# Optimization experiments

Hardware: AMD Instinct MI355X
Metric: run time of the kernel (lower is better)

The kernel has to match this reference:

```python
import jax, jax.numpy as jnp
import numpy as np

N, DEG, F_IN, F_OUT, H = 8192, 16, 1024, 128, 8


def setup_inputs() -> dict:
    key = jax.random.key(0)
    ks = jax.random.split(key, 6)
    features = jax.random.normal(ks[0], (N, F_IN), dtype=jnp.float32)
    adj = jax.random.randint(ks[1], (N, DEG), 0, N)  # fixed-degree adjacency
    W = jax.random.normal(ks[2], (H, F_IN, F_OUT), dtype=jnp.float32) / np.sqrt(F_IN)
    bW = jax.random.normal(ks[3], (H, F_OUT), dtype=jnp.float32) * 0.01
    a = jax.random.normal(ks[4], (H, 2 * F_OUT), dtype=jnp.float32) / np.sqrt(2.0 * F_OUT)
    ba = jax.random.normal(ks[5], (H,), dtype=jnp.float32) * 0.01
    return {"features": features, "adj": adj, "W": W, "bW": bW, "a": a, "ba": ba}


def reference(features, adj, W, bW, a, ba):
    n = features.shape[0]
    # neighbors with self appended last (matches adjlist[node] + [node])
    nbr = jnp.concatenate([adj, jnp.arange(n)[:, None]], axis=1)  # [N, DEG+1]
    # per-head linear transform: h[k] = features @ W_k + b_k
    h = jnp.einsum('nf,hfo->hno', features, W) + bW[:, None, :]  # [H, N, F_OUT]
    # attention score a_k([h_dst, h_src]) + bias decomposed into dst/src parts
    a_dst, a_src = a[:, :F_OUT], a[:, F_OUT:]
    s_dst = jnp.einsum('hno,ho->hn', h, a_dst)  # [H, N]
    s_src = jnp.einsum('hno,ho->hn', h, a_src)  # [H, N]
    scores = s_dst[:, :, None] + s_src[:, nbr] + ba[:, None, None]  # [H, N, DEG+1]
    scores = jax.nn.leaky_relu(scores, 0.2)
    alpha = jax.nn.softmax(scores, axis=-1)  # softmax over neighbors (incl. self)
    h_src = h[:, nbr]  # [H, N, DEG+1, F_OUT]
    out = jnp.einsum('hnd,hndf->hnf', alpha, h_src)  # [H, N, F_OUT]
    # concat heads along feature dim -> [N, H*F_OUT]
    return out.transpose(1, 0, 2).reshape(n, H * F_OUT)
```

## Files before the change

### kernel.cpp

```cpp
#include <hip/hip_runtime.h>
#include <hip/hip_bf16.h>

#define N_NODES 8192
#define DEG     16
#define F_IN    1024
#define F_OUT   128
#define NH      8

typedef __bf16 bf16x8 __attribute__((ext_vector_type(8)));
typedef float  f32x4  __attribute__((ext_vector_type(4)));

__device__ __forceinline__ float bf2f(unsigned short u) {
    union { unsigned int i; float f; } v;
    v.i = ((unsigned int)u) << 16;
    return v.f;
}
__device__ __forceinline__ unsigned short f2bf(float f) {
    union { float f; unsigned int u; } v; v.f = f;
    unsigned int u = v.u + 0x7FFFu + ((v.u >> 16) & 1u);
    return (unsigned short)(u >> 16);
}
__device__ __forceinline__ int detect_bf16(const unsigned int* __restrict__ w) {
    int hits = 0;
#pragma unroll
    for (int i = 0; i < 64; ++i) {
        unsigned int x = w[i * 131 + 17];
        int e = (x >> 7) & 0xFF;
        hits += (e >= 100 && e <= 140) ? 1 : 0;
    }
    return hits > 32;
}
__device__ __forceinline__ float rd_scalar(const void* p, int idx, int isbf) {
    return isbf ? bf2f(((const unsigned short*)p)[idx]) : ((const float*)p)[idx];
}
__device__ __forceinline__ void gload16(const void* g, void* l) {
    __builtin_amdgcn_global_load_lds(
        (const __attribute__((address_space(1))) void*)g,
        (__attribute__((address_space(3))) void*)l, 16, 0, 0);
}

__global__ __launch_bounds__(256) void prep_inputs(
    const void* __restrict__ feat, const void* __restrict__ W,
    unsigned short* __restrict__ featb, unsigned short* __restrict__ Wt)
{
    const int isbf = detect_bf16((const unsigned int*)feat);
    if (blockIdx.x < 4096) {
        size_t i8 = ((size_t)blockIdx.x * 256 + threadIdx.x) * 8;
        if (isbf) {
            *(uint4*)(featb + i8) = ((const uint4*)feat)[i8 / 8];
        } else {
            const float* s = (const float*)feat + i8;
            float4 u0 = *(const float4*)s;
            float4 u1 = *(const float4*)(s + 4);
            unsigned short t[8] = { f2bf(u0.x), f2bf(u0.y), f2bf(u0.z), f2bf(u0.w),
                                    f2bf(u1.x), f2bf(u1.y), f2bf(u1.z), f2bf(u1.w) };
            *(uint4*)(featb + i8) = *(const uint4*)t;
        }
    } else {
        __shared__ float tile[64][65];
        const int bx = blockIdx.x - 4096;
        const int h  = bx >> 5;
        const int kt = (bx >> 1) & 15;
        const int ot = bx & 1;
        const int t  = threadIdx.x;
#pragma unroll
        for (int i = 0; i < 16; ++i) {
            int id = i * 256 + t, r = id >> 6, c = id & 63;
            tile[r][c] = rd_scalar(W, ((h * 1024 + kt * 64 + r) * 128) + ot * 64 + c, isbf);
        }
        __syncthreads();
#pragma unroll
        for (int i = 0; i < 16; ++i) {
            int id = i * 256 + t, oc = id >> 6, kc = id & 63;
            Wt[(size_t)(h * 128 + ot * 64 + oc) * 1024 + kt * 64 + kc] = f2bf(tile[kc][oc]);
        }
    }
}

__global__ __launch_bounds__(512, 2) void gat_gemm4(
    const unsigned short* __restrict__ featb,
    const unsigned short* __restrict__ Wt,
    const void* __restrict__ raw_feat,
    const void* __restrict__ bW, const void* __restrict__ a,
    const void* __restrict__ ba,
    __hip_bfloat16* __restrict__ hbuf,
    float* __restrict__ sdst, float* __restrict__ ssrc)
{
    const int rawbf = detect_bf16((const unsigned int*)raw_feat);

    const int h   = blockIdx.y;
    const int n0  = blockIdx.x * 256;
    const int tid = threadIdx.x;

    __shared__ __align__(16) unsigned short As[3][256 * 64];
    __shared__ __align__(16) unsigned short Bs[3][128 * 64];
    __shared__ float sred[4][2][2][64];

    const int lane = tid & 63;
    const int wave = tid >> 6;
    const int wr   = wave >> 1;
    const int wc   = wave & 1;
    const int quad = lane >> 4;
    const int l16  = lane & 15;
    const int srow   = lane >> 3;
    const int schunk = lane & 7;

    f32x4 acc[4][4];
#pragma unroll
    for (int i = 0; i < 4; ++i)
#pragma unroll
        for (int j = 0; j < 4; ++j) acc[i][j] = (f32x4)0.f;

    const unsigned short* wbase = Wt + (size_t)h * F_OUT * F_IN;

    auto stage = [&](int kt, int s) {
        if (kt >= 16) return;
        const int kk0 = kt * 64;
#pragma unroll
        for (int t = 0; t < 4; ++t) {
            const int r0  = t * 64 + wave * 8;
            const int row = r0 + srow;
            const int gc  = schunk ^ (row & 7);
            gload16(&featb[(size_t)(n0 + row) * F_IN + kk0 + gc * 8],
                    &As[s][r0 * 64]);
        }
#pragma unroll
        for (int t = 0; t < 2; ++t) {
            const int r0  = t * 64 + wave * 8;
            const int row = r0 + srow;
            const int gc  = schunk ^ (row & 7);
            gload16(&wbase[(size_t)row * F_IN + kk0 + gc * 8],
                    &Bs[s][r0 * 64]);
        }
    };

    stage(0, 0);
    stage(1, 1);

    for (int t = 0; t < 16; ++t) {
        stage(t + 2, (t + 2) % 3);
        if (t < 14)       asm volatile("s_waitcnt vmcnt(12)" ::: "memory");
        else if (t == 14) asm volatile("s_waitcnt vmcnt(6)"  ::: "memory");
        else              asm volatile("s_waitcnt vmcnt(0)"  ::: "memory");
        asm volatile("s_barrier" ::: "memory");

        const unsigned short* Ab = As[t % 3];
        const unsigned short* Bb = Bs[t % 3];
#pragma unroll
        for (int ks = 0; ks < 2; ++ks) {
            const int kc = ks * 4 + quad;
            const int cs = (kc ^ (l16 & 7)) * 8;
            bf16x8 af[4], bfr[4];
#pragma unroll
            for (int rt = 0; rt < 4; ++rt)
                af[rt] = *(const bf16x8*)&Ab[(wr * 64 + rt * 16 + l16) * 64 + cs];
#pragma unroll
            for (int ct = 0; ct < 4; ++ct)
                bfr[ct] = *(const bf16x8*)&Bb[(wc * 64 + ct * 16 + l16) * 64 + cs];
            __builtin_amdgcn_s_setprio(1);
#pragma unroll
            for (int rt = 0; rt < 4; ++rt)
#pragma unroll
                for (int ct = 0; ct < 4; ++ct)
                    acc[rt][ct] = __builtin_amdgcn_mfma_f32_16x16x32_bf16(
                        af[rt], bfr[ct], acc[rt][ct], 0, 0, 0);
            __builtin_amdgcn_s_setprio(0);
        }
        asm volatile("s_barrier" ::: "memory");
    }

    float adst[4], asrc[4];
#pragma unroll
    for (int ct = 0; ct < 4; ++ct) {
        const int col = wc * 64 + ct * 16 + l16;
        adst[ct] = rd_scalar(a, h * 256 + col, rawbf);
        asrc[ct] = rd_scalar(a, h * 256 + 128 + col, rawbf);
    }
    float pd[4][4] = {}, ps[4][4] = {};
#pragma unroll
    for (int ct = 0; ct < 4; ++ct) {
        const int col = wc * 64 + ct * 16 + l16;
        const float bwv = rd_scalar(bW, h * F_OUT + col, rawbf);
#pragma unroll
        for (int rt = 0; rt < 4; ++rt) {
            const int nrow = n0 + wr * 64 + rt * 16 + quad * 4;
            __hip_bfloat16* dst = hbuf + ((size_t)h * N_NODES + nrow) * F_OUT + col;
#pragma unroll
            for (int r = 0; r < 4; ++r) {
                dst[(size_t)r * F_OUT] = __float2bfloat16(acc[rt][ct][r] + bwv);
                pd[rt][r] += acc[rt][ct][r] * adst[ct];
                ps[rt][r] += acc[rt][ct][r] * asrc[ct];
            }
        }
    }
#pragma unroll
    for (int off = 1; off < 16; off <<= 1)
#pragma unroll
        for (int rt = 0; rt < 4; ++rt)
#pragma unroll
            for (int r = 0; r < 4; ++r) {
                pd[rt][r] += __shfl_xor(pd[rt][r], off, 64);
                ps[rt][r] += __shfl_xor(ps[rt][r], off, 64);
            }
    if (l16 == 0) {
#pragma unroll
        for (int rt = 0; rt < 4; ++rt)
#pragma unroll
            for (int r = 0; r < 4; ++r) {
                const int row64 = rt * 16 + quad * 4 + r;
                sred[wr][wc][0][row64] = pd[rt][r];
                sred[wr][wc][1][row64] = ps[rt][r];
            }
    }
    __syncthreads();
    if (wc == 0) {
        const float bav = rd_scalar(ba, h, rawbf);
        const int row64 = lane;
        const float vd = sred[wr][0][0][row64] + sred[wr][1][0][row64] + bav;
        const float vs = sred[wr][0][1][row64] + sred[wr][1][1][row64];
        const int nrow = n0 + wr * 64 + row64;
        sdst[h * N_NODES + nrow] = vd;
        ssrc[h * N_NODES + nrow] = vs;
    }
}

__global__ __launch_bounds__(256) void gat_aggr4(
    const unsigned short* __restrict__ hbuf,
    const int* __restrict__ adj,
    const float* __restrict__ sdst, const float* __restrict__ ssrc,
    const void* __restrict__ raw_feat, void* __restrict__ out)
{
    const int isbf = detect_bf16((const unsigned int*)raw_feat);
    const int h    = blockIdx.x;
    const int wave = threadIdx.x >> 6;
    const int lane = threadIdx.x & 63;
    const int half = lane >> 5;
    const int l32  = lane & 31;
    const int n    = blockIdx.y * 8 + wave * 2 + half;

    int nbr = n;
    if (l32 < DEG) nbr = adj[n * DEG + l32];

    float s = -1e30f;
    if (l32 < 17) {
        float sv = sdst[h * N_NODES + n] + ssrc[h * N_NODES + nbr];
        s = sv > 0.f ? sv : 0.2f * sv;
    }
    float m = s;
#pragma unroll
    for (int off = 1; off < 32; off <<= 1)
        m = fmaxf(m, __shfl_xor(m, off, 64));
    float ev = (l32 < 17) ? __expf(s - m) : 0.f;
    float sum = ev;
#pragma unroll
    for (int off = 1; off < 32; off <<= 1)
        sum += __shfl_xor(sum, off, 64);
    ev *= (1.f / sum);

    const unsigned short* hb = hbuf + (size_t)h * N_NODES * F_OUT;
    const int fc    = l32 * 4;
    const int sbase = half << 5;
    float a0 = 0.f, a1 = 0.f, a2 = 0.f, a3 = 0.f;
#pragma unroll
    for (int d = 0; d < 17; ++d) {
        const int   nb = __shfl(nbr, sbase + d, 64);
        const float av = __shfl(ev,  sbase + d, 64);
        uint2 pk = *(const uint2*)&hb[(size_t)nb * F_OUT + fc];
        a0 += av * bf2f((unsigned short)(pk.x & 0xffffu));
        a1 += av * bf2f((unsigned short)(pk.x >> 16));
        a2 += av * bf2f((unsigned short)(pk.y & 0xffffu));
        a3 += av * bf2f((unsigned short)(pk.y >> 16));
    }

    const size_t oidx = (size_t)n * (NH * F_OUT) + h * F_OUT + fc;
    if (isbf) {
        uint2 res;
        res.x = (unsigned int)f2bf(a0) | ((unsigned int)f2bf(a1) << 16);
        res.y = (unsigned int)f2bf(a2) | ((unsigned int)f2bf(a3) << 16);
        *(uint2*)&((unsigned short*)out)[oidx] = res;
    } else {
        float4 res = { a0, a1, a2, a3 };
        *(float4*)&((float*)out)[oidx] = res;
    }
}

__global__ __launch_bounds__(256) void gat_gemm_fb(
    const void* __restrict__ feat, const void* __restrict__ W,
    const void* __restrict__ bW, __hip_bfloat16* __restrict__ hbuf)
{
    const int isbf = detect_bf16((const unsigned int*)feat);
    const int h = blockIdx.y, n0 = blockIdx.x * 128, tid = threadIdx.x;
    __shared__ __align__(16) unsigned short As[128][72];
    __shared__ __align__(16) unsigned short Bs[128][72];
    const int lane = tid & 63, wave = tid >> 6, quad = lane >> 4, l16 = lane & 15;
    f32x4 acc[2][8];
#pragma unroll
    for (int i = 0; i < 2; ++i)
#pragma unroll
        for (int j = 0; j < 8; ++j) acc[i][j] = (f32x4)0.f;
    for (int k0 = 0; k0 < F_IN; k0 += 64) {
        if (isbf) {
            const unsigned short* fbase = (const unsigned short*)feat + (size_t)n0 * F_IN;
            const unsigned short* wsrc  = (const unsigned short*)W +
                                          (size_t)h * F_IN * F_OUT + (size_t)k0 * F_OUT;
#pragma unroll
            for (int t = 0; t < 4; ++t) {
                int c = t * 256 + tid, row = c >> 3, kc = c & 7;
                *(uint4*)&As[row][kc * 8] = *(const uint4*)&fbase[row * F_IN + k0 + kc * 8];
            }
#pragma unroll
            for (int t = 0; t < 2; ++t) {
                int c = t * 256 + tid, kr2 = c >> 4, mm = c & 15, oc = mm * 8;
                uint4 w0 = *(const uint4*)&wsrc[(2 * kr2) * F_OUT + oc];
                uint4 w1 = *(const uint4*)&wsrc[(2 * kr2 + 1) * F_OUT + oc];
                const unsigned short* p0 = (const unsigned short*)&w0;
                const unsigned short* p1 = (const unsigned short*)&w1;
#pragma unroll
                for (int j = 0; j < 8; ++j) {
                    int i = (j + mm) & 7;
                    *(unsigned int*)&Bs[oc + i][2 * kr2] =
                        (unsigned int)p0[i] | ((unsigned int)p1[i] << 16);
                }
            }
        } else {
            const float* fbase = (const float*)feat + (size_t)n0 * F_IN;
            const float* wsrc  = (const float*)W +
                                 (size_t)h * F_IN * F_OUT + (size_t)k0 * F_OUT;
#pragma unroll
            for (int t = 0; t < 4; ++t) {
                int c = t * 256 + tid, row = c >> 3, kc = c & 7;
                const float* src = &fbase[row * F_IN + k0 + kc * 8];
                float4 u0 = *(const float4*)src, u1 = *(const float4*)(src + 4);
                unsigned short sh[8] = { f2bf(u0.x), f2bf(u0.y), f2bf(u0.z), f2bf(u0.w),
                                         f2bf(u1.x), f2bf(u1.y), f2bf(u1.z), f2bf(u1.w) };
                *(uint4*)&As[row][kc * 8] = *(const uint4*)sh;
            }
#pragma unroll
            for (int t = 0; t < 2; ++t) {
                int c = t * 256 + tid, kr2 = c >> 4, mm = c & 15, oc = mm * 8;
                const float* r0 = &wsrc[(2 * kr2) * F_OUT + oc];
                const float* r1 = &wsrc[(2 * kr2 + 1) * F_OUT + oc];
                float4 e0 = *(const float4*)r0, e1 = *(const float4*)(r0 + 4);
                float4 o0 = *(const float4*)r1, o1 = *(const float4*)(r1 + 4);
                unsigned short p0[8] = { f2bf(e0.x), f2bf(e0.y), f2bf(e0.z), f2bf(e0.w),
                                         f2bf(e1.x), f2bf(e1.y), f2bf(e1.z), f2bf(e1.w) };
                unsigned short p1[8] = { f2bf(o0.x), f2bf(o0.y), f2bf(o0.z), f2bf(o0.w),
                                         f2bf(o1.x), f2bf(o1.y), f2bf(o1.z), f2bf(o1.w) };
#pragma unroll
                for (int j = 0; j < 8; ++j) {
                    int i = (j + mm) & 7;
                    *(unsigned int*)&Bs[oc + i][2 * kr2] =
                        (unsigned int)p0[i] | ((unsigned int)p1[i] << 16);
                }
            }
        }
        __syncthreads();
#pragma unroll
        for (int ks = 0; ks < 2; ++ks) {
            const int kk = ks * 32 + quad * 8;
            bf16x8 af[2], bfr[8];
#pragma unroll
            for (int rt = 0; rt < 2; ++rt)
                af[rt] = *(const bf16x8*)&As[wave * 32 + rt * 16 + l16][kk];
#pragma unroll
            for (int ct = 0; ct < 8; ++ct)
                bfr[ct] = *(const bf16x8*)&Bs[ct * 16 + l16][kk];
#pragma unroll
            for (int rt = 0; rt < 2; ++rt)
#pragma unroll
                for (int ct = 0; ct < 8; ++ct)
                    acc[rt][ct] = __builtin_amdgcn_mfma_f32_16x16x32_bf16(
                        af[rt], bfr[ct], acc[rt][ct], 0, 0, 0);
        }
        __syncthreads();
    }
#pragma unroll
    for (int ct = 0; ct < 8; ++ct) {
        const int col = ct * 16 + l16;
        const float bwv = rd_scalar(bW, h * F_OUT + col, isbf);
#pragma unroll
        for (int rt = 0; rt < 2; ++rt) {
            const int nrow = n0 + wave * 32 + rt * 16 + quad * 4;
            __hip_bfloat16* dst = hbuf + ((size_t)h * N_NODES + nrow) * F_OUT + col;
#pragma unroll
            for (int r = 0; r < 4; ++r)
                dst[(size_t)r * F_OUT] = __float2bfloat16(acc[rt][ct][r] + bwv);
        }
    }
}

__global__ __launch_bounds__(256) void gat_aggr_fb(
    const __hip_bfloat16* __restrict__ hbuf, const int* __restrict__ adj,
    const void* __restrict__ a, const void* __restrict__ ba,
    void* __restrict__ out, const void* __restrict__ feat)
{
    const int isbf = detect_bf16((const unsigned int*)feat);
    const int n = blockIdx.x, wave = threadIdx.x >> 6, lane = threadIdx.x & 63;
    const int hh = blockIdx.y * 4 + wave;
    int nbr_reg = n;
    if (lane < DEG) nbr_reg = adj[n * DEG + lane];
    const int f0 = lane * 2;
    const float adst0 = rd_scalar(a, hh * 256 + f0, isbf);
    const float adst1 = rd_scalar(a, hh * 256 + f0 + 1, isbf);
    const float asrc0 = rd_scalar(a, hh * 256 + 128 + f0, isbf);
    const float asrc1 = rd_scalar(a, hh * 256 + 128 + f0 + 1, isbf);
    const float bav   = rd_scalar(ba, hh, isbf);
    const __hip_bfloat16* hb = hbuf + (size_t)hh * N_NODES * F_OUT;
    float v0[17], v1[17], red[18];
#pragma unroll
    for (int d = 0; d < 17; ++d) {
        int nb = __shfl(nbr_reg, d, 64);
        unsigned int pk = *(const unsigned int*)&hb[(size_t)nb * F_OUT + f0];
        v0[d] = bf2f((unsigned short)(pk & 0xffffu));
        v1[d] = bf2f((unsigned short)(pk >> 16));
        red[d] = v0[d] * asrc0 + v1[d] * asrc1;
    }
    red[17] = v0[16] * adst0 + v1[16] * adst1;
#pragma unroll
    for (int off = 1; off < 64; off <<= 1)
#pragma unroll
        for (int r = 0; r < 18; ++r) red[r] += __shfl_xor(red[r], off, 64);
    const float sd = red[17] + bav;
    float sc[17], mx = -1e30f;
#pragma unroll
    for (int d = 0; d < 17; ++d) {
        float s = sd + red[d];
        s = s > 0.f ? s : 0.2f * s;
        sc[d] = s; mx = fmaxf(mx, s);
    }
    float ssum = 0.f;
#pragma unroll
    for (int d = 0; d < 17; ++d) { sc[d] = __expf(sc[d] - mx); ssum += sc[d]; }
    const float inv = 1.f / ssum;
    float o0 = 0.f, o1 = 0.f;
#pragma unroll
    for (int d = 0; d < 17; ++d) { o0 += sc[d] * v0[d]; o1 += sc[d] * v1[d]; }
    o0 *= inv; o1 *= inv;
    const size_t oidx = (size_t)n * (NH * F_OUT) + hh * F_OUT + f0;
    if (isbf) {
        *(unsigned int*)&((unsigned short*)out)[oidx] =
            (unsigned int)f2bf(o0) | ((unsigned int)f2bf(o1) << 16);
    } else {
        float2 res; res.x = o0; res.y = o1;
        *(float2*)&((float*)out)[oidx] = res;
    }
}

extern "C" void kernel_launch(void* const* d_in, const int* in_sizes, int n_in,
                              void* d_out, int out_size, void* d_ws, size_t ws_size,
                              hipStream_t stream)
{
    const void* feat = d_in[0];
    const int*  adj  = (const int*)d_in[1];
    const void* W    = d_in[2];
    const void* bW   = d_in[3];
    const void* a    = d_in[4];
    const void* ba   = d_in[5];

    char* ws = (char*)d_ws;
    __hip_bfloat16* hbuf = (__hip_bfloat16*)ws;
    const size_t HB = (size_t)NH * N_NODES * F_OUT * 2;
    const size_t SC = (size_t)NH * N_NODES * 4;
    float* sdst = (float*)(ws + HB);
    float* ssrc = (float*)(ws + HB + SC);
    unsigned short* featb = (unsigned short*)(ws + HB + 2 * SC);
    unsigned short* Wt    = featb + (size_t)N_NODES * F_IN;
    const size_t needA = HB + 2 * SC +
        ((size_t)N_NODES * F_IN + (size_t)NH * F_IN * F_OUT) * 2;

    if (ws_size >= needA) {
        prep_inputs<<<4352, 256, 0, stream>>>(feat, W, featb, Wt);
        gat_gemm4<<<dim3(32, 8), 512, 0, stream>>>(featb, Wt, feat, bW, a, ba,
                                                   hbuf, sdst, ssrc);
        gat_aggr4<<<dim3(8, 1024), 256, 0, stream>>>((const unsigned short*)hbuf,
                                                     adj, sdst, ssrc, feat, d_out);
    } else {
        gat_gemm_fb<<<dim3(64, 8), 256, 0, stream>>>(feat, W, bW, hbuf);
        gat_aggr_fb<<<dim3(8192, 2), 256, 0, stream>>>(hbuf, adj, a, ba, d_out, feat);
    }
}
```

Measured before the change: 157.0 us.

## Rework GEMM mainloop into double-buffered, interleaved load/MFMA phases with block remap

```diff
diff --git a/kernel.cpp b/kernel.cpp
--- a/kernel.cpp
+++ b/kernel.cpp
@@ -77,7 +77,7 @@
     }
 }
 
-__global__ __launch_bounds__(512, 2) void gat_gemm4(
+__global__ __launch_bounds__(512, 2) void gat_gemm8(
     const unsigned short* __restrict__ featb,
     const unsigned short* __restrict__ Wt,
     const void* __restrict__ raw_feat,
@@ -89,12 +89,13 @@
     const int rawbf = detect_bf16((const unsigned int*)raw_feat);
 
     const int h   = blockIdx.y;
-    const int n0  = blockIdx.x * 256;
+    const int bx  = blockIdx.x;
+    const int bxp = ((bx & 7) << 2) | (bx >> 3);
+    const int n0  = bxp * 256;
     const int tid = threadIdx.x;
 
-    __shared__ __align__(16) unsigned short As[3][256 * 64];
-    __shared__ __align__(16) unsigned short Bs[3][128 * 64];
-    __shared__ float sred[4][2][2][64];
+    __shared__ __align__(16) unsigned short As[2][256 * 64];
+    __shared__ __align__(16) unsigned short Bs[2][128 * 64];
 
     const int lane = tid & 63;
     const int wave = tid >> 6;
@@ -102,6 +103,7 @@
     const int wc   = wave & 1;
     const int quad = lane >> 4;
     const int l16  = lane & 15;
+    const int sw   = l16 & 7;
     const int srow   = lane >> 3;
     const int schunk = lane & 7;
 
@@ -113,60 +115,118 @@
 
     const unsigned short* wbase = Wt + (size_t)h * F_OUT * F_IN;
 
-    auto stage = [&](int kt, int s) {
-        if (kt >= 16) return;
-        const int kk0 = kt * 64;
-#pragma unroll
-        for (int t = 0; t < 4; ++t) {
-            const int r0  = t * 64 + wave * 8;
-            const int row = r0 + srow;
-            const int gc  = schunk ^ (row & 7);
-            gload16(&featb[(size_t)(n0 + row) * F_IN + kk0 + gc * 8],
-                    &As[s][r0 * 64]);
-        }
-#pragma unroll
-        for (int t = 0; t < 2; ++t) {
-            const int r0  = t * 64 + wave * 8;
-            const int row = r0 + srow;
-            const int gc  = schunk ^ (row & 7);
-            gload16(&wbase[(size_t)row * F_IN + kk0 + gc * 8],
-                    &Bs[s][r0 * 64]);
-        }
+    auto stageA = [&](int kt, int s, int r) {
+        const int r0  = r * 64 + wave * 8;
+        const int row = r0 + srow;
+        const int gc  = schunk ^ (row & 7);
+        gload16(&featb[(size_t)(n0 + row) * F_IN + kt * 64 + gc * 8],
+                &As[s][r0 * 64]);
     };
-
-    stage(0, 0);
-    stage(1, 1);
+    auto stageB = [&](int kt, int s, int r) {
+        const int r0  = r * 64 + wave * 8;
+        const int row = r0 + srow;
+        const int gc  = schunk ^ (row & 7);
+        gload16(&wbase[(size_t)row * F_IN + kt * 64 + gc * 8],
+                &Bs[s][r0 * 64]);
+    };
+
+    stageA(0, 0, 0); stageA(0, 0, 1); stageA(0, 0, 2); stageA(0, 0, 3);
+    stageB(0, 0, 0); stageB(0, 0, 1);
 
     for (int t = 0; t < 16; ++t) {
-        stage(t + 2, (t + 2) % 3);
-        if (t < 14)       asm volatile("s_waitcnt vmcnt(12)" ::: "memory");
-        else if (t == 14) asm volatile("s_waitcnt vmcnt(6)"  ::: "memory");
-        else              asm volatile("s_waitcnt vmcnt(0)"  ::: "memory");
+        const int cur = t & 1;
+        const int nxt = cur ^ 1;
+        bf16x8 af[4], b0, b1;
+
         asm volatile("s_barrier" ::: "memory");
-
-        const unsigned short* Ab = As[t % 3];
-        const unsigned short* Bb = Bs[t % 3];
-#pragma unroll
-        for (int ks = 0; ks < 2; ++ks) {
-            const int kc = ks * 4 + quad;
-            const int cs = (kc ^ (l16 & 7)) * 8;
-            bf16x8 af[4], bfr[4];
-#pragma unroll
-            for (int rt = 0; rt < 4; ++rt)
-                af[rt] = *(const bf16x8*)&Ab[(wr * 64 + rt * 16 + l16) * 64 + cs];
-#pragma unroll
-            for (int ct = 0; ct < 4; ++ct)
-                bfr[ct] = *(const bf16x8*)&Bb[(wc * 64 + ct * 16 + l16) * 64 + cs];
+        if (t < 15) {
+            stageA(t + 1, nxt, 0); stageA(t + 1, nxt, 1);
+            asm volatile("s_waitcnt vmcnt(2)" ::: "memory");
+        } else {
+            asm volatile("s_waitcnt vmcnt(0)" ::: "memory");
+        }
+        asm volatile("s_barrier" ::: "memory");
+        {
+            const int cs = (quad ^ sw) * 8;
+#pragma unroll
+            for (int rt = 0; rt < 4; ++rt)
+                af[rt] = *(const bf16x8*)&As[cur][(wr * 64 + rt * 16 + l16) * 64 + cs];
+            b0 = *(const bf16x8*)&Bs[cur][(wc * 64 + 0 * 16 + l16) * 64 + cs];
+            b1 = *(const bf16x8*)&Bs[cur][(wc * 64 + 1 * 16 + l16) * 64 + cs];
             __builtin_amdgcn_s_setprio(1);
 #pragma unroll
             for (int rt = 0; rt < 4; ++rt)
-#pragma unroll
-                for (int ct = 0; ct < 4; ++ct)
-                    acc[rt][ct] = __builtin_amdgcn_mfma_f32_16x16x32_bf16(
-                        af[rt], bfr[ct], acc[rt][ct], 0, 0, 0);
+                acc[rt][0] = __builtin_amdgcn_mfma_f32_16x16x32_bf16(af[rt], b0, acc[rt][0], 0, 0, 0);
+#pragma unroll
+            for (int rt = 0; rt < 4; ++rt)
+                acc[rt][1] = __builtin_amdgcn_mfma_f32_16x16x32_bf16(af[rt], b1, acc[rt][1], 0, 0, 0);
             __builtin_amdgcn_s_setprio(0);
         }
+
+        if (t < 15) { stageA(t + 1, nxt, 2); stageA(t + 1, nxt, 3); }
         asm volatile("s_barrier" ::: "memory");
+        {
+            const int cs = (quad ^ sw) * 8;
+            b0 = *(const bf16x8*)&Bs[cur][(wc * 64 + 2 * 16 + l16) * 64 + cs];
+            b1 = *(const bf16x8*)&Bs[cur][(wc * 64 + 3 * 16 + l16) * 64 + cs];
+            __builtin_amdgcn_s_setprio(1);
+#pragma unroll
+            for (int rt = 0; rt < 4; ++rt)
+                acc[rt][2] = __builtin_amdgcn_mfma_f32_16x16x32_bf16(af[rt], b0, acc[rt][2], 0, 0, 0);
+#pragma unroll
+            for (int rt = 0; rt < 4; ++rt)
+                acc[rt][3] = __builtin_amdgcn_mfma_f32_16x16x32_bf16(af[rt], b1, acc[rt][3], 0, 0, 0);
+            __builtin_amdgcn_s_setprio(0);
+        }
+
+        if (t < 15) { stageB(t + 1, nxt, 0); stageB(t + 1, nxt, 1); }
+        asm volatile("s_barrier" ::: "memory");
+        {
+            const int cs = ((4 + quad) ^ sw) * 8;
+#pragma unroll
+            for (int rt = 0; rt < 4; ++rt)
+                af[rt] = *(const bf16x8*)&As[cur][(wr * 64 + rt * 16 + l16) * 64 + cs];
+            b0 = *(const bf16x8*)&Bs[cur][(wc * 64 + 0 * 16 + l16) * 64 + cs];
+            b1 = *(const bf16x8*)&Bs[cur][(wc * 64 + 1 * 16 + l16) * 64 + cs];
+            __builtin_amdgcn_s_setprio(1);
+#pragma unroll
+            for (int rt = 0; rt < 4; ++rt)
+                acc[rt][0] = __builtin_amdgcn_mfma_f32_16x16x32_bf16(af[rt], b0, acc[rt][0], 0, 0, 0);
+#pragma unroll
+            for (int rt = 0; rt < 4; ++rt)
+                acc[rt][1] = __builtin_amdgcn_mfma_f32_16x16x32_bf16(af[rt], b1, acc[rt][1], 0, 0, 0);
+            __builtin_amdgcn_s_setprio(0);
+        }
+
+        asm volatile("s_barrier" ::: "memory");
+        {
+            const int cs = ((4 + quad) ^ sw) * 8;
+            b0 = *(const bf16x8*)&Bs[cur][(wc * 64 + 2 * 16 + l16) * 64 + cs];
+            b1 = *(const bf16x8*)&Bs[cur][(wc * 64 + 3 * 16 + l16) * 64 + cs];
+            __builtin_amdgcn_s_setprio(1);
+#pragma unroll
+            for (int rt = 0; rt < 4; ++rt)
+                acc[rt][2] = __builtin_amdgcn_mfma_f32_16x16x32_bf16(af[rt], b0, acc[rt][2], 0, 0, 0);
+#pragma unroll
+            for (int rt = 0; rt < 4; ++rt)
+                acc[rt][3] = __builtin_amdgcn_mfma_f32_16x16x32_bf16(af[rt], b1, acc[rt][3], 0, 0, 0);
+            __builtin_amdgcn_s_setprio(0);
+        }
+    }
+    __syncthreads();
+
+#pragma unroll
+    for (int ct = 0; ct < 4; ++ct) {
+        const int col = wc * 64 + ct * 16 + l16;
+        const float bwv = rd_scalar(bW, h * F_OUT + col, rawbf);
+#pragma unroll
+        for (int rt = 0; rt < 4; ++rt) {
+            const int nrow = n0 + wr * 64 + rt * 16 + quad * 4;
+            __hip_bfloat16* dst = hbuf + ((size_t)h * N_NODES + nrow) * F_OUT + col;
+#pragma unroll
+            for (int r = 0; r < 4; ++r)
+                dst[(size_t)r * F_OUT] = __float2bfloat16(acc[rt][ct][r] + bwv);
+        }
     }
 
     float adst[4], asrc[4];
@@ -178,21 +238,14 @@
     }
     float pd[4][4] = {}, ps[4][4] = {};
 #pragma unroll
-    for (int ct = 0; ct < 4; ++ct) {
-        const int col = wc * 64 + ct * 16 + l16;
-        const float bwv = rd_scalar(bW, h * F_OUT + col, rawbf);
-#pragma unroll
-        for (int rt = 0; rt < 4; ++rt) {
-            const int nrow = n0 + wr * 64 + rt * 16 + quad * 4;
-            __hip_bfloat16* dst = hbuf + ((size_t)h * N_NODES + nrow) * F_OUT + col;
+    for (int rt = 0; rt < 4; ++rt)
+#pragma unroll
+        for (int ct = 0; ct < 4; ++ct)
 #pragma unroll
             for (int r = 0; r < 4; ++r) {
-                dst[(size_t)r * F_OUT] = __float2bfloat16(acc[rt][ct][r] + bwv);
                 pd[rt][r] += acc[rt][ct][r] * adst[ct];
                 ps[rt][r] += acc[rt][ct][r] * asrc[ct];
             }
-        }
-    }
 #pragma unroll
     for (int off = 1; off < 16; off <<= 1)
 #pragma unroll
@@ -202,23 +255,26 @@
                 pd[rt][r] += __shfl_xor(pd[rt][r], off, 64);
                 ps[rt][r] += __shfl_xor(ps[rt][r], off, 64);
             }
+
+    float* sred = (float*)&As[0][0];
     if (l16 == 0) {
 #pragma unroll
         for (int rt = 0; rt < 4; ++rt)
 #pragma unroll
             for (int r = 0; r < 4; ++r) {
                 const int row64 = rt * 16 + quad * 4 + r;
-                sred[wr][wc][0][row64] = pd[rt][r];
-                sred[wr][wc][1][row64] = ps[rt][r];
+                sred[((wr * 2 + wc) * 2 + 0) * 64 + row64] = pd[rt][r];
+                sred[((wr * 2 + wc) * 2 + 1) * 64 + row64] = ps[rt][r];
             }
     }
     __syncthreads();
     if (wc == 0) {
         const float bav = rd_scalar(ba, h, rawbf);
-        const int row64 = lane;
-        const float vd = sred[wr][0][0][row64] + sred[wr][1][0][row64] + bav;
-        const float vs = sred[wr][0][1][row64] + sred[wr][1][1][row64];
-        const int nrow = n0 + wr * 64 + row64;
+        const float vd = sred[((wr * 2 + 0) * 2 + 0) * 64 + lane]
+                       + sred[((wr * 2 + 1) * 2 + 0) * 64 + lane] + bav;
+        const float vs = sred[((wr * 2 + 0) * 2 + 1) * 64 + lane]
+                       + sred[((wr * 2 + 1) * 2 + 1) * 64 + lane];
+        const int nrow = n0 + wr * 64 + lane;
         sdst[h * N_NODES + nrow] = vd;
         ssrc[h * N_NODES + nrow] = vs;
     }
@@ -470,7 +526,7 @@
 
     if (ws_size >= needA) {
         prep_inputs<<<4352, 256, 0, stream>>>(feat, W, featb, Wt);
-        gat_gemm4<<<dim3(32, 8), 512, 0, stream>>>(featb, Wt, feat, bW, a, ba,
+        gat_gemm8<<<dim3(32, 8), 512, 0, stream>>>(featb, Wt, feat, bW, a, ba,
                                                    hbuf, sdst, ssrc);
         gat_aggr4<<<dim3(8, 1024), 256, 0, stream>>>((const unsigned short*)hbuf,
                                                      adj, sdst, ssrc, feat, d_out);
```

Result: no change. 157.7 us (+0.5%).
